# Kernel optimization log

Hardware: AMD Instinct MI355X
Metric: run time of the kernel (lower is better)

The kernel has to match this reference:

```python
import jax, jax.numpy as jnp
import numpy as np

N_EMBD = 1024
N_HEAD = 16
B, T = 2, 2048
LN_EPS = 1e-5


def _linear_params(key, d_in, d_out):
    k1, k2 = jax.random.split(key)
    bound = 1.0 / np.sqrt(d_in)
    W = jax.random.uniform(k1, (d_in, d_out), jnp.float32, -bound, bound)
    b = jax.random.uniform(k2, (d_out,), jnp.float32, -bound, bound)
    return W, b


def setup_inputs() -> dict:
    key = jax.random.key(0)
    ks = jax.random.split(key, 8)
    x = jax.random.normal(ks[0], (B, T, N_EMBD), jnp.float32)
    Wq, bq = _linear_params(ks[1], N_EMBD, N_EMBD)
    Wk, bk = _linear_params(ks[2], N_EMBD, N_EMBD)
    Wv, bv = _linear_params(ks[3], N_EMBD, N_EMBD)
    Wo, bo = _linear_params(ks[4], N_EMBD, N_EMBD)
    W1, b1 = _linear_params(ks[5], N_EMBD, 4 * N_EMBD)
    W2, b2 = _linear_params(ks[6], 4 * N_EMBD, N_EMBD)
    ln1_g = jnp.ones((N_EMBD,), jnp.float32)
    ln1_b = jnp.zeros((N_EMBD,), jnp.float32)
    ln2_g = jnp.ones((N_EMBD,), jnp.float32)
    ln2_b = jnp.zeros((N_EMBD,), jnp.float32)
    return dict(x=x, Wq=Wq, bq=bq, Wk=Wk, bk=bk, Wv=Wv, bv=bv, Wo=Wo, bo=bo,
                W1=W1, b1=b1, W2=W2, b2=b2,
                ln1_g=ln1_g, ln1_b=ln1_b, ln2_g=ln2_g, ln2_b=ln2_b)


def _layernorm(x, g, b):
    mu = jnp.mean(x, axis=-1, keepdims=True)
    var = jnp.mean(jnp.square(x - mu), axis=-1, keepdims=True)
    return (x - mu) * jax.lax.rsqrt(var + LN_EPS) * g + b


def _attention(x, Wq, bq, Wk, bk, Wv, bv, Wo, bo):
    Bsz, Tlen, C = x.shape
    hd = C // N_HEAD
    q = (x @ Wq + bq).reshape(Bsz, Tlen, N_HEAD, hd)
    k = (x @ Wk + bk).reshape(Bsz, Tlen, N_HEAD, hd)
    v = (x @ Wv + bv).reshape(Bsz, Tlen, N_HEAD, hd)
    scale = 1.0 / np.sqrt(hd)
    # NOTE: the original module's mask buffer is all ones -> masked_fill is a
    # no-op, so attention is FULL (non-causal) despite the class name.
    att = jnp.einsum('bqhd,bkhd->bhqk', q, k) * scale
    att = jax.nn.softmax(att, axis=-1)
    y = jnp.einsum('bhqk,bkhd->bqhd', att, v).reshape(Bsz, Tlen, C)
    return y @ Wo + bo


def reference(x, Wq, bq, Wk, bk, Wv, bv, Wo, bo, W1, b1, W2, b2,
              ln1_g, ln1_b, ln2_g, ln2_b):
    x = x + _attention(_layernorm(x, ln1_g, ln1_b), Wq, bq, Wk, bk, Wv, bv, Wo, bo)
    h = _layernorm(x, ln2_g, ln2_b)
    h = jax.nn.gelu(h @ W1 + b1, approximate=False) @ W2 + b2
    return x + h
```

## Files before the change

kernel.cpp:

```cpp
#include <hip/hip_runtime.h>
#include <hip/hip_bf16.h>
#include <math.h>


typedef __bf16 bf16x8 __attribute__((ext_vector_type(8)));
typedef float f32x4 __attribute__((ext_vector_type(4)));

__device__ __forceinline__ unsigned short f2bf(float f) {
  union { float f; unsigned int u; } v; v.f = f;
  unsigned int u = v.u;
  unsigned int r = (u + 0x7fffu + ((u >> 16) & 1u)) >> 16;
  return (unsigned short)r;
}

__device__ __forceinline__ unsigned int fbits(float f) {
  union { float f; unsigned int u; } v; v.f = f;
  return v.u;
}

__device__ __forceinline__ bf16x8 ld_bf16x8(const unsigned short* p) {
  union { uint4 u; bf16x8 v; } x;
  x.u = *(const uint4*)p;
  return x.v;
}

__device__ __forceinline__ void async_copy16(const void* g, void* l) {
  __builtin_amdgcn_global_load_lds(
      (const __attribute__((address_space(1))) void*)g,
      (__attribute__((address_space(3))) void*)l, 16, 0, 0);
}

__global__ __launch_bounds__(256) void transpose_cast_kernel(
    const float* __restrict__ W, unsigned short* __restrict__ Wt, int N, int K) {
  __shared__ unsigned short tile[32][33];
  const int n0 = blockIdx.x * 32, k0 = blockIdx.y * 32;
  const int t = threadIdx.x;
  const int r = t >> 3, cq = (t & 7) * 4;
  float4 v = *(const float4*)&W[(size_t)(k0 + r) * N + n0 + cq];
  tile[cq + 0][r] = f2bf(v.x);
  tile[cq + 1][r] = f2bf(v.y);
  tile[cq + 2][r] = f2bf(v.z);
  tile[cq + 3][r] = f2bf(v.w);
  __syncthreads();
  ushort4 o;
  o.x = tile[r][cq + 0];
  o.y = tile[r][cq + 1];
  o.z = tile[r][cq + 2];
  o.w = tile[r][cq + 3];
  *(ushort4*)&Wt[(size_t)(n0 + r) * K + k0 + cq] = o;
}

__global__ __launch_bounds__(256) void transpose_v_kernel(
    const unsigned short* __restrict__ V, unsigned short* __restrict__ Vt) {
  __shared__ unsigned short tile[32][36];
  const int kt = blockIdx.x * 32;
  const int d0 = blockIdx.y * 32;
  const int bh = blockIdx.z;
  const int bb = bh >> 4, h = bh & 15;
  const int t = threadIdx.x;
  const int r = t >> 3, c4 = (t & 7) * 4;
  ushort4 v = *(const ushort4*)&V[((size_t)bb * 2048 + kt + r) * 1024 + h * 64 + d0 + c4];
  tile[c4 + 0][r] = v.x;
  tile[c4 + 1][r] = v.y;
  tile[c4 + 2][r] = v.z;
  tile[c4 + 3][r] = v.w;
  __syncthreads();
  ushort4 o;
  o.x = tile[r][c4 + 0];
  o.y = tile[r][c4 + 1];
  o.z = tile[r][c4 + 2];
  o.w = tile[r][c4 + 3];
  *(ushort4*)&Vt[((size_t)bh * 64 + d0 + r) * 2048 + kt + c4] = o;
}

__global__ __launch_bounds__(256) void ln_kernel(
    const float* __restrict__ x, const float* __restrict__ g,
    const float* __restrict__ b, unsigned short* __restrict__ out) {
  const int row = blockIdx.x, t = threadIdx.x;
  const float4 v = ((const float4*)(x + (size_t)row * 1024))[t];
  float s = v.x + v.y + v.z + v.w;
  float s2 = v.x * v.x + v.y * v.y + v.z * v.z + v.w * v.w;
  for (int o = 32; o > 0; o >>= 1) {
    s += __shfl_xor(s, o, 64);
    s2 += __shfl_xor(s2, o, 64);
  }
  __shared__ float red[8];
  const int w = t >> 6;
  if ((t & 63) == 0) { red[w] = s; red[4 + w] = s2; }
  __syncthreads();
  s = red[0] + red[1] + red[2] + red[3];
  s2 = red[4] + red[5] + red[6] + red[7];
  const float mu = s * (1.f / 1024.f);
  const float var = s2 * (1.f / 1024.f) - mu * mu;
  const float rs = rsqrtf(var + 1e-5f);
  const float4 gg = ((const float4*)g)[t];
  const float4 bb = ((const float4*)b)[t];
  ushort4 o4;
  o4.x = f2bf((v.x - mu) * rs * gg.x + bb.x);
  o4.y = f2bf((v.y - mu) * rs * gg.y + bb.y);
  o4.z = f2bf((v.z - mu) * rs * gg.z + bb.z);
  o4.w = f2bf((v.w - mu) * rs * gg.w + bb.w);
  ((ushort4*)(out + (size_t)row * 1024))[t] = o4;
}

enum { MODE_QKV = 0, MODE_RES = 1, MODE_GELU = 2 };

#define QSCALE 0.18033688011112043f

template <int BM, int BN, int MODE>
__global__ __launch_bounds__(256) void gemm_kernel(
    const unsigned short* __restrict__ A, const unsigned short* __restrict__ Bt,
    const float* __restrict__ bias0, const float* __restrict__ bias1,
    const float* __restrict__ bias2, const float* __restrict__ residual,
    void* __restrict__ out0, void* __restrict__ out1, void* __restrict__ out2,
    int M, int N, int K) {
  constexpr int MI = BM / 32;
  constexpr int NI = BN / 32;
  __shared__ __align__(16) unsigned short As[2][2][BM * 32];
  __shared__ __align__(16) unsigned short Bs[2][2][BN * 32];
  const int t = threadIdx.x;

  const int NT = N / BN;
  const int NTX = NT >> 3;
  const int bid = blockIdx.x;
  const int xcd = bid & 7, local = bid >> 3;
  const int nt_ = xcd * NTX + local % NTX;
  const int mt = local / NTX;
  const int m0 = mt * BM, n0 = nt_ * BN;

  const int l = t & 63, w = t >> 6;
  const int wm = (w >> 1) * (BM / 2), wn = (w & 1) * (BN / 2);
  const int lr = l & 15, lq = l >> 4;

  f32x4 acc[MI][NI];
#pragma unroll
  for (int i = 0; i < MI; i++)
#pragma unroll
    for (int j = 0; j < NI; j++) {
      f32x4 z = {0.f, 0.f, 0.f, 0.f};
      acc[i][j] = z;
    }

  auto issue = [&](int k0, int p) {
#pragma unroll
    for (int h = 0; h < 2; h++)
#pragma unroll
      for (int s = 0; s < BM / 64; s++) {
        const int c = t + s * 256;
        const int row = c >> 2, k8 = (c & 3) * 8;
        async_copy16(&A[(size_t)(m0 + row) * K + k0 + h * 32 + k8],
                     &As[p][h][c * 8]);
      }
#pragma unroll
    for (int h = 0; h < 2; h++)
#pragma unroll
      for (int s = 0; s < BN / 64; s++) {
        const int c = t + s * 256;
        const int row = c >> 2, k8 = (c & 3) * 8;
        async_copy16(&Bt[(size_t)(n0 + row) * K + k0 + h * 32 + k8],
                     &Bs[p][h][c * 8]);
      }
  };

  issue(0, 0);
  int p = 0;
  for (int k0 = 0; k0 < K; k0 += 64) {
    __syncthreads();
    if (k0 + 64 < K) issue(k0 + 64, p ^ 1);
#pragma unroll
    for (int kk = 0; kk < 2; kk++) {
      bf16x8 af[MI], bf[NI];
#pragma unroll
      for (int mi = 0; mi < MI; mi++)
        af[mi] = ld_bf16x8(&As[p][kk][(wm + mi * 16 + lr) * 32 + lq * 8]);
#pragma unroll
      for (int ni = 0; ni < NI; ni++)
        bf[ni] = ld_bf16x8(&Bs[p][kk][(wn + ni * 16 + lr) * 32 + lq * 8]);
#pragma unroll
      for (int mi = 0; mi < MI; mi++)
#pragma unroll
        for (int ni = 0; ni < NI; ni++)
          acc[mi][ni] = __builtin_amdgcn_mfma_f32_16x16x32_bf16(
              af[mi], bf[ni], acc[mi][ni], 0, 0, 0);
    }
    p ^= 1;
  }

#pragma unroll
  for (int mi = 0; mi < MI; mi++) {
#pragma unroll
    for (int ni = 0; ni < NI; ni++) {
#pragma unroll
      for (int i = 0; i < 4; i++) {
        const int gm = m0 + wm + mi * 16 + lq * 4 + i;
        const int gn = n0 + wn + ni * 16 + lr;
        const float v = acc[mi][ni][i];
        if (MODE == MODE_QKV) {
          const int sel = gn >> 10, cn = gn & 1023;
          const float* bb = sel == 0 ? bias0 : (sel == 1 ? bias1 : bias2);
          unsigned short* dst =
              (unsigned short*)(sel == 0 ? out0 : (sel == 1 ? out1 : out2));
          float u = v + bb[cn];
          if (sel == 0) u *= QSCALE;
          dst[(size_t)gm * 1024 + cn] = f2bf(u);
        } else if (MODE == MODE_RES) {
          ((float*)out0)[(size_t)gm * N + gn] =
              v + bias0[gn] + residual[(size_t)gm * N + gn];
        } else {
          const float u = v + bias0[gn];
          const float ge = 0.5f * u * (1.f + erff(u * 0.70710678118654752f));
          ((unsigned short*)out0)[(size_t)gm * N + gn] = f2bf(ge);
        }
      }
    }
  }
}

__global__ __launch_bounds__(256) void attn_kernel(
    const unsigned short* __restrict__ Q, const unsigned short* __restrict__ Kt,
    const unsigned short* __restrict__ Vt, unsigned short* __restrict__ O) {
  __shared__ __align__(16) unsigned short QPs[128 * 72];
  __shared__ __align__(16) unsigned short Ks[64 * 72];
  __shared__ __align__(16) unsigned short Vs[64 * 72];
  const int qt = blockIdx.x;
  const int bh = blockIdx.y;
  const int bb = bh >> 4, h = bh & 15;
  const int t = threadIdx.x, l = t & 63, w = t >> 6;
  const int lr = l & 15, lq = l >> 4;
  const size_t rowBase = (size_t)bb * 2048;
  const int col0 = h * 64;

#pragma unroll
  for (int s = 0; s < 4; s++) {
    const int c = t + s * 256;
    const int r = c >> 3, c8 = (c & 7) * 8;
    *(uint4*)&QPs[r * 72 + c8] =
        *(const uint4*)&Q[(rowBase + qt * 128 + r) * 1024 + col0 + c8];
  }
  __syncthreads();
  bf16x8 qf[2][2];
#pragma unroll
  for (int s = 0; s < 2; s++)
#pragma unroll
    for (int kk = 0; kk < 2; kk++)
      qf[s][kk] = ld_bf16x8(&QPs[(w * 32 + s * 16 + lr) * 72 + kk * 32 + lq * 8]);

  f32x4 oacc[2][4];
#pragma unroll
  for (int s = 0; s < 2; s++)
#pragma unroll
    for (int nt = 0; nt < 4; nt++) {
      f32x4 z = {0.f, 0.f, 0.f, 0.f};
      oacc[s][nt] = z;
    }
  float lp[2] = {0.f, 0.f};

  for (int kt = 0; kt < 2048; kt += 64) {
    __syncthreads();
#pragma unroll
    for (int s = 0; s < 2; s++) {
      const int c = t + s * 256;
      const int r = c >> 3, c8 = (c & 7) * 8;
      *(uint4*)&Ks[r * 72 + c8] =
          *(const uint4*)&Kt[(rowBase + kt + r) * 1024 + col0 + c8];
      *(uint4*)&Vs[r * 72 + c8] =
          *(const uint4*)&Vt[((size_t)bh * 64 + r) * 2048 + kt + c8];
    }
    __syncthreads();

    f32x4 st[2][4];
#pragma unroll
    for (int s = 0; s < 2; s++)
#pragma unroll
      for (int nt = 0; nt < 4; nt++) {
        f32x4 z = {0.f, 0.f, 0.f, 0.f};
        st[s][nt] = z;
      }
#pragma unroll
    for (int nt = 0; nt < 4; nt++)
#pragma unroll
      for (int kk = 0; kk < 2; kk++) {
        bf16x8 kf = ld_bf16x8(&Ks[(nt * 16 + lr) * 72 + kk * 32 + lq * 8]);
        st[0][nt] = __builtin_amdgcn_mfma_f32_16x16x32_bf16(kf, qf[0][kk], st[0][nt], 0, 0, 0);
        st[1][nt] = __builtin_amdgcn_mfma_f32_16x16x32_bf16(kf, qf[1][kk], st[1][nt], 0, 0, 0);
      }

#pragma unroll
    for (int s = 0; s < 2; s++) {
      float rsum = 0.f;
#pragma unroll
      for (int nt = 0; nt < 4; nt++)
#pragma unroll
        for (int i = 0; i < 4; i++) {
          const float p = exp2f(st[s][nt][i]);
          st[s][nt][i] = p;
          rsum += p;
        }
      lp[s] += rsum;
    }

#pragma unroll
    for (int s = 0; s < 2; s++)
#pragma unroll
      for (int nt = 0; nt < 4; nt++) {
        uint2 pk;
        pk.x = __builtin_amdgcn_perm(fbits(st[s][nt][1]), fbits(st[s][nt][0]), 0x07060302u);
        pk.y = __builtin_amdgcn_perm(fbits(st[s][nt][3]), fbits(st[s][nt][2]), 0x07060302u);
        *(uint2*)&QPs[(w * 32 + s * 16 + lr) * 72 + nt * 16 + lq * 4] = pk;
      }

#pragma unroll
    for (int kb = 0; kb < 2; kb++) {
      bf16x8 pf0 = ld_bf16x8(&QPs[(w * 32 + lr) * 72 + kb * 32 + lq * 8]);
      bf16x8 pf1 = ld_bf16x8(&QPs[(w * 32 + 16 + lr) * 72 + kb * 32 + lq * 8]);
#pragma unroll
      for (int nt = 0; nt < 4; nt++) {
        bf16x8 vf = ld_bf16x8(&Vs[(nt * 16 + lr) * 72 + kb * 32 + lq * 8]);
        oacc[0][nt] = __builtin_amdgcn_mfma_f32_16x16x32_bf16(pf0, vf, oacc[0][nt], 0, 0, 0);
        oacc[1][nt] = __builtin_amdgcn_mfma_f32_16x16x32_bf16(pf1, vf, oacc[1][nt], 0, 0, 0);
      }
    }
  }

#pragma unroll
  for (int s = 0; s < 2; s++) {
    float li = lp[s];
    li += __shfl_xor(li, 16, 64);
    li += __shfl_xor(li, 32, 64);
    const float inv = 1.f / li;
#pragma unroll
    for (int nt = 0; nt < 4; nt++)
#pragma unroll
      for (int i = 0; i < 4; i++) {
        const size_t orow = rowBase + qt * 128 + w * 32 + s * 16 + lq * 4 + i;
        const int ocol = col0 + nt * 16 + lr;
        O[orow * 1024 + ocol] = f2bf(oacc[s][nt][i] * inv);
      }
  }
}

extern "C" void kernel_launch(void* const* d_in, const int* in_sizes, int n_in,
                              void* d_out, int out_size, void* d_ws, size_t ws_size,
                              hipStream_t stream) {
  const float* x    = (const float*)d_in[0];
  const float* Wq   = (const float*)d_in[1];
  const float* bq   = (const float*)d_in[2];
  const float* Wk   = (const float*)d_in[3];
  const float* bk   = (const float*)d_in[4];
  const float* Wv   = (const float*)d_in[5];
  const float* bv   = (const float*)d_in[6];
  const float* Wo   = (const float*)d_in[7];
  const float* bo   = (const float*)d_in[8];
  const float* W1   = (const float*)d_in[9];
  const float* b1   = (const float*)d_in[10];
  const float* W2   = (const float*)d_in[11];
  const float* b2   = (const float*)d_in[12];
  const float* ln1g = (const float*)d_in[13];
  const float* ln1b = (const float*)d_in[14];
  const float* ln2g = (const float*)d_in[15];
  const float* ln2b = (const float*)d_in[16];

  char* ws = (char*)d_ws;
  const size_t MB = 1024ull * 1024ull;
  unsigned short* WqT = (unsigned short*)(ws + 0 * MB);
  unsigned short* WkT = (unsigned short*)(ws + 2 * MB);
  unsigned short* WvT = (unsigned short*)(ws + 4 * MB);
  unsigned short* WoT = (unsigned short*)(ws + 6 * MB);
  unsigned short* W1T = (unsigned short*)(ws + 8 * MB);
  unsigned short* W2T = (unsigned short*)(ws + 16 * MB);
  unsigned short* xn  = (unsigned short*)(ws + 24 * MB);
  unsigned short* Qb  = (unsigned short*)(ws + 32 * MB);
  unsigned short* Kb  = (unsigned short*)(ws + 40 * MB);
  unsigned short* Vb  = (unsigned short*)(ws + 48 * MB);
  unsigned short* Ob  = (unsigned short*)(ws + 56 * MB);
  float*          x1  = (float*)(ws + 64 * MB);
  unsigned short* h2  = (unsigned short*)(ws + 80 * MB);
  unsigned short* VtG = (unsigned short*)(ws + 24 * MB);
  unsigned short* Hb  = (unsigned short*)(ws + 24 * MB);

  const dim3 blk(256);

  transpose_cast_kernel<<<dim3(32, 32), blk, 0, stream>>>(Wq, WqT, 1024, 1024);
  transpose_cast_kernel<<<dim3(32, 32), blk, 0, stream>>>(Wk, WkT, 1024, 1024);
  transpose_cast_kernel<<<dim3(32, 32), blk, 0, stream>>>(Wv, WvT, 1024, 1024);
  transpose_cast_kernel<<<dim3(32, 32), blk, 0, stream>>>(Wo, WoT, 1024, 1024);
  transpose_cast_kernel<<<dim3(128, 32), blk, 0, stream>>>(W1, W1T, 4096, 1024);
  transpose_cast_kernel<<<dim3(32, 128), blk, 0, stream>>>(W2, W2T, 1024, 4096);

  ln_kernel<<<4096, blk, 0, stream>>>(x, ln1g, ln1b, xn);

  gemm_kernel<128, 128, MODE_QKV><<<dim3(24 * 32), blk, 0, stream>>>(
      xn, WqT, bq, bk, bv, nullptr, Qb, Kb, Vb, 4096, 3072, 1024);

  transpose_v_kernel<<<dim3(64, 2, 32), blk, 0, stream>>>(Vb, VtG);

  attn_kernel<<<dim3(16, 32), blk, 0, stream>>>(Qb, Kb, VtG, Ob);

  gemm_kernel<64, 128, MODE_RES><<<dim3(8 * 64), blk, 0, stream>>>(
      Ob, WoT, bo, nullptr, nullptr, x, x1, nullptr, nullptr, 4096, 1024, 1024);

  ln_kernel<<<4096, blk, 0, stream>>>(x1, ln2g, ln2b, h2);

  gemm_kernel<128, 128, MODE_GELU><<<dim3(32 * 32), blk, 0, stream>>>(
      h2, W1T, b1, nullptr, nullptr, nullptr, Hb, nullptr, nullptr, 4096, 4096, 1024);

  gemm_kernel<64, 128, MODE_RES><<<dim3(8 * 64), blk, 0, stream>>>(
      Hb, W2T, b2, nullptr, nullptr, x1, (float*)d_out, nullptr, nullptr, 4096, 1024, 4096);
}
```

Before: 424.2 us.

## Double-buffer K/V tiles in attention with register prefetch and XCD-aware block mapping

The attention kernel now prefetches the next K/V tile into registers while computing on the current one, writing it into a second LDS buffer so each iteration needs one barrier instead of two. Blocks are remapped on a 1D grid so that all blocks for a given (batch, head) land on the same XCD, improving L2 reuse of K/V. It also uses the hardware exp2 builtin, batches V fragment loads ahead of the MFMAs, and raises wave priority around the MFMA groups. The costs are doubled K/V LDS and extra registers for the prefetch, which may lower occupancy.

```diff
diff --git a/kernel.cpp b/kernel.cpp
--- a/kernel.cpp
+++ b/kernel.cpp
@@ -22,6 +22,14 @@
   union { uint4 u; bf16x8 v; } x;
   x.u = *(const uint4*)p;
   return x.v;
+}
+
+__device__ __forceinline__ float fast_exp2(float x) {
+#if __has_builtin(__builtin_amdgcn_exp2f)
+  return __builtin_amdgcn_exp2f(x);
+#else
+  return exp2f(x);
+#endif
 }
 
 __device__ __forceinline__ void async_copy16(const void* g, void* l) {
@@ -220,16 +228,41 @@
     const unsigned short* __restrict__ Q, const unsigned short* __restrict__ Kt,
     const unsigned short* __restrict__ Vt, unsigned short* __restrict__ O) {
   __shared__ __align__(16) unsigned short QPs[128 * 72];
-  __shared__ __align__(16) unsigned short Ks[64 * 72];
-  __shared__ __align__(16) unsigned short Vs[64 * 72];
-  const int qt = blockIdx.x;
-  const int bh = blockIdx.y;
+  __shared__ __align__(16) unsigned short Ks[2][64 * 72];
+  __shared__ __align__(16) unsigned short Vs[2][64 * 72];
+  const int id = blockIdx.x;
+  const int xcd = id & 7, loc = id >> 3;
+  const int bh = xcd * 4 + (loc >> 4);
+  const int qt = loc & 15;
   const int bb = bh >> 4, h = bh & 15;
   const int t = threadIdx.x, l = t & 63, w = t >> 6;
   const int lr = l & 15, lq = l >> 4;
   const size_t rowBase = (size_t)bb * 2048;
   const int col0 = h * 64;
 
+  const int sr = t >> 3;
+  const int sc8 = (t & 7) * 8;
+
+  uint4 kreg[2], vreg[2];
+  auto issue_kv = [&](int kt) {
+#pragma unroll
+    for (int s = 0; s < 2; s++) {
+      const int r = sr + s * 32;
+      kreg[s] = *(const uint4*)&Kt[(rowBase + kt + r) * 1024 + col0 + sc8];
+      vreg[s] = *(const uint4*)&Vt[((size_t)bh * 64 + r) * 2048 + kt + sc8];
+    }
+  };
+  auto write_kv = [&](int p) {
+#pragma unroll
+    for (int s = 0; s < 2; s++) {
+      const int r = sr + s * 32;
+      *(uint4*)&Ks[p][r * 72 + sc8] = kreg[s];
+      *(uint4*)&Vs[p][r * 72 + sc8] = vreg[s];
+    }
+  };
+
+  issue_kv(0);
+
 #pragma unroll
   for (int s = 0; s < 4; s++) {
     const int c = t + s * 256;
@@ -245,6 +278,10 @@
     for (int kk = 0; kk < 2; kk++)
       qf[s][kk] = ld_bf16x8(&QPs[(w * 32 + s * 16 + lr) * 72 + kk * 32 + lq * 8]);
 
+  write_kv(0);
+  issue_kv(64);
+  __syncthreads();
+
   f32x4 oacc[2][4];
 #pragma unroll
   for (int s = 0; s < 2; s++)
@@ -255,18 +292,12 @@
     }
   float lp[2] = {0.f, 0.f};
 
+  int p = 0;
   for (int kt = 0; kt < 2048; kt += 64) {
-    __syncthreads();
-#pragma unroll
-    for (int s = 0; s < 2; s++) {
-      const int c = t + s * 256;
-      const int r = c >> 3, c8 = (c & 7) * 8;
-      *(uint4*)&Ks[r * 72 + c8] =
-          *(const uint4*)&Kt[(rowBase + kt + r) * 1024 + col0 + c8];
-      *(uint4*)&Vs[r * 72 + c8] =
-          *(const uint4*)&Vt[((size_t)bh * 64 + r) * 2048 + kt + c8];
-    }
-    __syncthreads();
+    if (kt + 64 < 2048) {
+      write_kv(p ^ 1);
+      if (kt + 128 < 2048) issue_kv(kt + 128);
+    }
 
     f32x4 st[2][4];
 #pragma unroll
@@ -277,13 +308,16 @@
         st[s][nt] = z;
       }
 #pragma unroll
-    for (int nt = 0; nt < 4; nt++)
-#pragma unroll
-      for (int kk = 0; kk < 2; kk++) {
-        bf16x8 kf = ld_bf16x8(&Ks[(nt * 16 + lr) * 72 + kk * 32 + lq * 8]);
-        st[0][nt] = __builtin_amdgcn_mfma_f32_16x16x32_bf16(kf, qf[0][kk], st[0][nt], 0, 0, 0);
-        st[1][nt] = __builtin_amdgcn_mfma_f32_16x16x32_bf16(kf, qf[1][kk], st[1][nt], 0, 0, 0);
-      }
+    for (int nt = 0; nt < 4; nt++) {
+      bf16x8 kf0 = ld_bf16x8(&Ks[p][(nt * 16 + lr) * 72 + 0 * 32 + lq * 8]);
+      bf16x8 kf1 = ld_bf16x8(&Ks[p][(nt * 16 + lr) * 72 + 1 * 32 + lq * 8]);
+      __builtin_amdgcn_s_setprio(1);
+      st[0][nt] = __builtin_amdgcn_mfma_f32_16x16x32_bf16(kf0, qf[0][0], st[0][nt], 0, 0, 0);
+      st[1][nt] = __builtin_amdgcn_mfma_f32_16x16x32_bf16(kf0, qf[1][0], st[1][nt], 0, 0, 0);
+      st[0][nt] = __builtin_amdgcn_mfma_f32_16x16x32_bf16(kf1, qf[0][1], st[0][nt], 0, 0, 0);
+      st[1][nt] = __builtin_amdgcn_mfma_f32_16x16x32_bf16(kf1, qf[1][1], st[1][nt], 0, 0, 0);
+      __builtin_amdgcn_s_setprio(0);
+    }
 
 #pragma unroll
     for (int s = 0; s < 2; s++) {
@@ -292,9 +326,9 @@
       for (int nt = 0; nt < 4; nt++)
 #pragma unroll
         for (int i = 0; i < 4; i++) {
-          const float p = exp2f(st[s][nt][i]);
-          st[s][nt][i] = p;
-          rsum += p;
+          const float pv = fast_exp2(st[s][nt][i]);
+          st[s][nt][i] = pv;
+          rsum += pv;
         }
       lp[s] += rsum;
     }
@@ -313,13 +347,21 @@
     for (int kb = 0; kb < 2; kb++) {
       bf16x8 pf0 = ld_bf16x8(&QPs[(w * 32 + lr) * 72 + kb * 32 + lq * 8]);
       bf16x8 pf1 = ld_bf16x8(&QPs[(w * 32 + 16 + lr) * 72 + kb * 32 + lq * 8]);
+      bf16x8 vf[4];
+#pragma unroll
+      for (int nt = 0; nt < 4; nt++)
+        vf[nt] = ld_bf16x8(&Vs[p][(nt * 16 + lr) * 72 + kb * 32 + lq * 8]);
+      __builtin_amdgcn_s_setprio(1);
 #pragma unroll
       for (int nt = 0; nt < 4; nt++) {
-        bf16x8 vf = ld_bf16x8(&Vs[(nt * 16 + lr) * 72 + kb * 32 + lq * 8]);
-        oacc[0][nt] = __builtin_amdgcn_mfma_f32_16x16x32_bf16(pf0, vf, oacc[0][nt], 0, 0, 0);
-        oacc[1][nt] = __builtin_amdgcn_mfma_f32_16x16x32_bf16(pf1, vf, oacc[1][nt], 0, 0, 0);
-      }
-    }
+        oacc[0][nt] = __builtin_amdgcn_mfma_f32_16x16x32_bf16(pf0, vf[nt], oacc[0][nt], 0, 0, 0);
+        oacc[1][nt] = __builtin_amdgcn_mfma_f32_16x16x32_bf16(pf1, vf[nt], oacc[1][nt], 0, 0, 0);
+      }
+      __builtin_amdgcn_s_setprio(0);
+    }
+
+    __syncthreads();
+    p ^= 1;
   }
 
 #pragma unroll
@@ -394,7 +436,7 @@
 
   transpose_v_kernel<<<dim3(64, 2, 32), blk, 0, stream>>>(Vb, VtG);
 
-  attn_kernel<<<dim3(16, 32), blk, 0, stream>>>(Qb, Kb, VtG, Ob);
+  attn_kernel<<<dim3(512), blk, 0, stream>>>(Qb, Kb, VtG, Ob);
 
   gemm_kernel<64, 128, MODE_RES><<<dim3(8 * 64), blk, 0, stream>>>(
       Ob, WoT, bo, nullptr, nullptr, x, x1, nullptr, nullptr, 4096, 1024, 1024);
```

Result: faster. 411.8 us (-2.9%).
